# Optimization experiments

Hardware: AMD Instinct MI355X
Metric: run time of the kernel (lower is better)

## Reference

```python
import jax, jax.numpy as jnp
import numpy as np

N = 50000; E = 800000; G = 64
HID = 128; HEADS = 4; HC = HID // HEADS
L = 3; RESID_FREQ = 2
EPS = 1e-5; SLOPE = 0.2


def setup_inputs() -> dict:
    key = jax.random.key(0)
    ks = jax.random.split(key, 16)
    s = 1.0 / np.sqrt(HID)
    f = jnp.float32
    return {
        "x": jax.random.normal(ks[0], (N, HID), f),
        "edge_index": jax.random.randint(ks[1], (2, E), 0, N, dtype=jnp.int32),
        "batch": jnp.sort(jax.random.randint(ks[2], (N,), 0, G, dtype=jnp.int32)),
        "w_in1": jax.random.normal(ks[3], (HID, HID), f) * s,
        "b_in1": jnp.zeros((HID,), f),
        "w_in2": jax.random.normal(ks[4], (HID, HID), f) * s,
        "b_in2": jnp.zeros((HID,), f),
        "gat_w": jax.random.normal(ks[5], (L, HID, HID), f) * s,
        "gat_att_src": jax.random.normal(ks[6], (L, HEADS, HC), f) * s,
        "gat_att_dst": jax.random.normal(ks[7], (L, HEADS, HC), f) * s,
        "gat_b": jnp.zeros((L, HID), f),
        "gcn_w": jax.random.normal(ks[8], (L, HID, HID), f) * s,
        "gcn_b": jnp.zeros((L, HID), f),
        "norm_w": jnp.ones((L, HID), f),
        "norm_b": jnp.zeros((L, HID), f),
        "norm_ms": jnp.ones((L, HID), f),
        "skip_w": jax.random.normal(ks[9], (L, HID, HID), f) * s,
        "skip_b": jnp.zeros((L, HID), f),
        "w_h1": jax.random.normal(ks[10], (HID, HID), f) * s,
        "b_h1": jnp.zeros((HID,), f),
        "w_h2": jax.random.normal(ks[11], (HID, HID // 2), f) * s,
        "b_h2": jnp.zeros((HID // 2,), f),
        "w_h3": jax.random.normal(ks[12], (HID // 2, 1), f) * s,
        "b_h3": jnp.zeros((1,), f),
        "edge_w_param": jnp.ones((1,), f),
    }


def _gat(x, src, dst, w, a_src, a_dst, b):
    # PyG GATConv (eval): lin -> per-edge additive attention -> edge softmax over dst -> scatter-sum
    h = (x @ w).reshape(N, HEADS, HC)
    sc_src = jnp.sum(h * a_src, axis=-1)  # [N, H]
    sc_dst = jnp.sum(h * a_dst, axis=-1)
    alpha = jax.nn.leaky_relu(sc_src[src] + sc_dst[dst], SLOPE)  # [Ef, H]
    amax = jax.ops.segment_max(alpha, dst, num_segments=N)  # every node has a self-loop
    ex = jnp.exp(alpha - amax[dst])
    denom = jax.ops.segment_sum(ex, dst, num_segments=N)
    coef = ex / (denom[dst] + 1e-16)
    out = jax.ops.segment_sum(h[src] * coef[:, :, None], dst, num_segments=N)
    return out.reshape(N, HID) + b


def _gcn(x, src, dst, ew, w, b):
    # PyG GCNConv with improved=True (self-loop weight 2.0 already in ew): sym-normalized SpMM
    deg = jax.ops.segment_sum(ew, dst, num_segments=N)
    dinv = jnp.where(deg > 0, jax.lax.rsqrt(deg), 0.0)
    norm = dinv[src] * ew * dinv[dst]
    h = x @ w
    return jax.ops.segment_sum(h[src] * norm[:, None], dst, num_segments=N) + b


def _graph_norm(x, batch, w, b, ms):
    cnt = jax.ops.segment_sum(jnp.ones((N, 1), x.dtype), batch, num_segments=G)
    cnt = jnp.maximum(cnt, 1.0)
    mean = jax.ops.segment_sum(x, batch, num_segments=G) / cnt
    out = x - mean[batch] * ms
    var = jax.ops.segment_sum(out * out, batch, num_segments=G) / cnt
    return out / jnp.sqrt(var[batch] + EPS) * w + b


def reference(x, edge_index, batch, w_in1, b_in1, w_in2, b_in2, gat_w, gat_att_src,
              gat_att_dst, gat_b, gcn_w, gcn_b, norm_w, norm_b, norm_ms, skip_w,
              skip_b, w_h1, b_h1, w_h2, b_h2, w_h3, b_h3, edge_w_param):
    # undirected: concat reversed edges; then self-loops (added by both GAT and GCN convs)
    loop = jnp.arange(N, dtype=edge_index.dtype)
    src = jnp.concatenate([edge_index[0], edge_index[1], loop])
    dst = jnp.concatenate([edge_index[1], edge_index[0], loop])
    ew = jnp.concatenate([
        edge_w_param[0] * jnp.ones((2 * E,), x.dtype),
        2.0 * jnp.ones((N,), x.dtype),  # improved=True self-loop fill value
    ])
    h = jax.nn.relu(x @ w_in1 + b_in1) @ w_in2 + b_in2
    for i in range(L):
        prev = h
        g1 = _gat(h, src, dst, gat_w[i], gat_att_src[i], gat_att_dst[i], gat_b[i])
        g2 = _gcn(h, src, dst, ew, gcn_w[i], gcn_b[i])
        h = jax.nn.elu(_graph_norm(g1 + g2, batch, norm_w[i], norm_b[i], norm_ms[i]))
        if i % RESID_FREQ == 0:
            h = h + prev @ skip_w[i] + skip_b[i]
    p = jax.nn.relu(h @ w_h1 + b_h1)
    p = jax.nn.relu(p @ w_h2 + b_h2)
    return jax.nn.sigmoid(p @ w_h3 + b_h3).reshape(-1)
```

## Files before the change

kernel.cpp:

```cpp
#include <hip/hip_runtime.h>
#include <hip/hip_fp16.h>

typedef unsigned int uint;
typedef unsigned short ushort;
typedef __attribute__((ext_vector_type(8))) short short8;
typedef __attribute__((ext_vector_type(4))) float f32x4;
typedef __attribute__((ext_vector_type(2))) float f32x2;

#define N_NODES 50000
#define N_EDGES 800000
#define ETOT    (2 * N_EDGES + N_NODES)
#define NG      64
#define NBKT    256
#define MAXB    10240
#define EPB     8192
#define NBK1    ((ETOT + EPB - 1) / EPB)
#define AROW    640

__device__ __forceinline__ short f2bf(float f) {
  uint u = __float_as_uint(f);
  u += 0x7fffu + ((u >> 16) & 1u);
  return (short)(u >> 16);
}
__device__ __forceinline__ float bf2f(short s) {
  return __uint_as_float(((uint)(ushort)s) << 16);
}
__device__ __forceinline__ uint packbf(float a, float b) {
  return (uint)(ushort)f2bf(a) | ((uint)(ushort)f2bf(b) << 16);
}
__device__ __forceinline__ uint pkh2(float a, float b) {
  __half2 h = __floats2half2_rn(a, b);
  return *(uint*)&h;
}
__device__ __forceinline__ float2 uph2(uint u) {
  __half2 h = *(__half2*)&u;
  return __half22float2(h);
}

__global__ __launch_bounds__(256) void bucket_k(const int* __restrict__ ei,
                                                int* __restrict__ gfill,
                                                uint* __restrict__ est) {
  __shared__ int hist[NBKT];
  __shared__ int cursor[NBKT];
  const int tid = threadIdx.x;
  hist[tid] = 0;
  __syncthreads();
  const int e0 = blockIdx.x * EPB;
#pragma unroll 4
  for (int i = 0; i < EPB / 256; ++i) {
    int e = e0 + i * 256 + tid;
    if (e < ETOT) {
      int d;
      if (e < N_EDGES)          d = ei[N_EDGES + e];
      else if (e < 2 * N_EDGES) d = ei[e - N_EDGES];
      else                      d = e - 2 * N_EDGES;
      atomicAdd(&hist[d >> 8], 1);
    }
  }
  __syncthreads();
  cursor[tid] = atomicAdd(&gfill[tid], hist[tid]);
  __syncthreads();
#pragma unroll 4
  for (int i = 0; i < EPB / 256; ++i) {
    int e = e0 + i * 256 + tid;
    if (e < ETOT) {
      int s, d, fl = 0;
      if (e < N_EDGES)          { s = ei[e];           d = ei[N_EDGES + e]; }
      else if (e < 2 * N_EDGES) { s = ei[e];           d = ei[e - N_EDGES]; }
      else                      { s = e - 2 * N_EDGES; d = s; fl = 1; }
      int b = d >> 8;
      int slot = atomicAdd(&cursor[b], 1);
      est[(size_t)b * MAXB + slot] = (uint)s | ((uint)(d & 255) << 16) | ((uint)fl << 24);
    }
  }
}

__global__ __launch_bounds__(256) void bktscan_k(const int* __restrict__ gfill,
                                                 int* __restrict__ bktbase) {
  __shared__ int wsum[4];
  int tid = threadIdx.x, lane = tid & 63, wid = tid >> 6;
  int v = gfill[tid];
  int x = v;
#pragma unroll
  for (int d = 1; d < 64; d <<= 1) {
    int t = __shfl_up(x, d, 64);
    if (lane >= d) x += t;
  }
  if (lane == 63) wsum[wid] = x;
  __syncthreads();
  int woff = 0;
#pragma unroll
  for (int j = 0; j < 4; ++j) if (j < wid) woff += wsum[j];
  bktbase[tid] = woff + x - v;
}

__global__ __launch_bounds__(256) void group_k(const int* __restrict__ gfill,
                                               const int* __restrict__ bktbase,
                                               const uint* __restrict__ est,
                                               const float* __restrict__ ewp,
                                               int* __restrict__ csrc,
                                               int* __restrict__ rbeg,
                                               int* __restrict__ rend,
                                               float* __restrict__ dinv) {
  __shared__ int hist[NBKT];
  __shared__ int cursor[NBKT];
  __shared__ int wsum[4];
  const int b = blockIdx.x;
  const int tid = threadIdx.x;
  const int cnt = gfill[b];
  const int gb = bktbase[b];
  hist[tid] = 0;
  __syncthreads();
  const uint* basep = est + (size_t)b * MAXB;
  for (int i = tid; i < cnt; i += 256)
    atomicAdd(&hist[(basep[i] >> 16) & 255], 1);
  __syncthreads();
  int v = hist[tid];
  int lane = tid & 63, wid = tid >> 6;
  int x = v;
#pragma unroll
  for (int d = 1; d < 64; d <<= 1) {
    int t = __shfl_up(x, d, 64);
    if (lane >= d) x += t;
  }
  if (lane == 63) wsum[wid] = x;
  __syncthreads();
  int woff = 0;
#pragma unroll
  for (int j = 0; j < 4; ++j) if (j < wid) woff += wsum[j];
  int excl = woff + x - v;
  cursor[tid] = excl;
  int node = b * 256 + tid;
  if (node < N_NODES) {
    rbeg[node] = gb + excl;
    rend[node] = gb + excl + v;
    float deg = ewp[0] * (float)(v - 1) + 2.0f;
    dinv[node] = (deg > 0.f) ? rsqrtf(deg) : 0.f;
  }
  __syncthreads();
  for (int i = tid; i < cnt; i += 256) {
    uint en = basep[i];
    int dlow = (en >> 16) & 255;
    int slot = atomicAdd(&cursor[dlow], 1);
    csrc[gb + slot] = (int)(en & 0xffffu) | (int)((en >> 24) << 31);
  }
}

__global__ __launch_bounds__(128) void gcnt_k(const int* __restrict__ batch,
                                              int* __restrict__ gcnt) {
  __shared__ int lb[NG + 1];
  int g = threadIdx.x;
  if (g <= NG) {
    int lo = 0, hi = N_NODES;
    while (lo < hi) {
      int mid = (lo + hi) >> 1;
      if (batch[mid] < g) lo = mid + 1; else hi = mid;
    }
    lb[g] = lo;
  }
  __syncthreads();
  if (g < NG) gcnt[g] = lb[g + 1] - lb[g];
}

__global__ __launch_bounds__(256) void convx_k(const float* __restrict__ x,
                                               short* __restrict__ xb) {
  int i = (blockIdx.x * 256 + threadIdx.x) * 4;
  float4 v = *(const float4*)(x + i);
  *(uint2*)(xb + i) = make_uint2(packbf(v.x, v.y), packbf(v.z, v.w));
}

__global__ __launch_bounds__(256) void prep_k(const float* __restrict__ w_in1,
                                              const float* __restrict__ w_in2,
                                              const float* __restrict__ gat_w,
                                              const float* __restrict__ gcn_w,
                                              const float* __restrict__ skip_w,
                                              const float* __restrict__ w_h1,
                                              const float* __restrict__ w_h2,
                                              short* __restrict__ WT0,
                                              short* __restrict__ WT1,
                                              short* __restrict__ WTL2,
                                              short* __restrict__ WTS,
                                              short* __restrict__ WTH1,
                                              short* __restrict__ WTH2) {
  int mat = blockIdx.x >> 2, qr = blockIdx.x & 3;
  const float* src; short* dst; int ncol = 128, dstride = 128, doff = 0;
  switch (mat) {
    case 0:  src = w_in1; dst = WT0; break;
    case 1:  src = w_in2; dst = WT1; break;
    case 2: case 3: case 4:
      src = gat_w + (size_t)(mat - 2) * 16384; dst = WTL2 + (size_t)(mat - 2) * 32768;
      dstride = 256; break;
    case 5: case 6: case 7:
      src = gcn_w + (size_t)(mat - 5) * 16384; dst = WTL2 + (size_t)(mat - 5) * 32768;
      dstride = 256; doff = 128; break;
    case 8:  src = skip_w;             dst = WTS;         break;
    case 9:  src = skip_w + 2 * 16384; dst = WTS + 16384; break;
    case 10: src = w_h1; dst = WTH1; break;
    default: src = w_h2; dst = WTH2; ncol = 64; break;
  }
  int total = 128 * ncol, chunk = total / 4;
  for (int d = qr * chunk + threadIdx.x; d < (qr + 1) * chunk; d += 256) {
    int col = d >> 7, k = d & 127;
    dst[col * dstride + doff + k] = f2bf(src[k * ncol + col]);
  }
}

__global__ __launch_bounds__(256) void attprep_k(const float* __restrict__ gat_w,
                                                 const float* __restrict__ asrc,
                                                 const float* __restrict__ adst,
                                                 const float* __restrict__ gat_b,
                                                 const float* __restrict__ gcn_b,
                                                 short* __restrict__ ATTW,
                                                 float* __restrict__ BSUM) {
  const int tid = threadIdx.x;
  for (int t = tid; t < 3072; t += 256) {
    int l = t >> 10, rem = t & 1023;
    int r = rem >> 7, k = rem & 127;
    int hd = r & 3;
    const float* av = (r < 4) ? (asrc + l * 128 + hd * 32) : (adst + l * 128 + hd * 32);
    const float* wrow = gat_w + (size_t)l * 16384 + k * 128 + hd * 32;
    float s = 0.f;
#pragma unroll
    for (int c = 0; c < 32; ++c) s = fmaf(wrow[c], av[c], s);
    ATTW[(size_t)l * 2048 + r * 128 + k] = f2bf(s);
  }
  for (int t = tid; t < 3072; t += 256)
    ATTW[(size_t)(t >> 10) * 2048 + 1024 + (t & 1023)] = 0;
  for (int t = tid; t < 384; t += 256) {
    int l = t >> 7, c = t & 127;
    BSUM[t] = gat_b[l * 128 + c] + gcn_b[l * 128 + c];
  }
}

template <int NCOL, int RELU, int ADD, int F32OUT>
__global__ __launch_bounds__(256) void bgemm_k(const short* __restrict__ A,
                                               const short* __restrict__ WT,
                                               const float* __restrict__ bias,
                                               const short* __restrict__ addsrc,
                                               short* __restrict__ outb,
                                               float* __restrict__ outf, int M) {
  constexpr int NT = NCOL / 16;
  const int lane = threadIdx.x & 63;
  const int wid = threadIdx.x >> 6;
  const int mbase = blockIdx.x * 64 + wid * 16;
  const int l15 = lane & 15, q = lane >> 4;
  int arow = mbase + l15; if (arow > M - 1) arow = M - 1;
  const short* ap = A + (size_t)arow * 128 + q * 8;
  const short* bp = WT + (size_t)l15 * 128 + q * 8;
  f32x4 acc[NT];
#pragma unroll
  for (int t = 0; t < NT; ++t) acc[t] = (f32x4)0.f;
#pragma unroll
  for (int c = 0; c < 4; ++c) {
    short8 av = *(const short8*)(ap + c * 32);
#pragma unroll
    for (int t = 0; t < NT; ++t) {
      short8 bv = *(const short8*)(bp + (size_t)t * 16 * 128 + c * 32);
      acc[t] = __builtin_amdgcn_mfma_f32_16x16x32_bf16(av, bv, acc[t], 0, 0, 0);
    }
  }
#pragma unroll
  for (int t = 0; t < NT; ++t) {
    int col = t * 16 + l15;
    float bb = bias ? bias[col] : 0.f;
#pragma unroll
    for (int r = 0; r < 4; ++r) {
      int row = mbase + q * 4 + r;
      if (row < M) {
        float v = acc[t][r] + bb;
        if (ADD) v += bf2f(addsrc[(size_t)row * 128 + col]);
        if (RELU) v = v > 0.f ? v : 0.f;
        if (F32OUT) outf[(size_t)row * NCOL + col] = v;
        else        outb[(size_t)row * NCOL + col] = f2bf(v);
      }
    }
  }
}

__global__ __launch_bounds__(256) void agg_k(const short* __restrict__ h,
                                             const float* __restrict__ sc,
                                             const int* __restrict__ rbeg,
                                             const int* __restrict__ rend,
                                             const int* __restrict__ cs,
                                             const float* __restrict__ dinv,
                                             const float* __restrict__ ewp,
                                             short* __restrict__ A) {
  __shared__ uint4 lco[4][64];
  const int n = blockIdx.x * 4 + (threadIdx.x >> 6);
  const int wv = threadIdx.x >> 6;
  const int l = threadIdx.x & 63;
  const int sub = l >> 5;
  const int f4 = l & 31;
  const float ew0 = ewp[0];
  const float dn = dinv[n];
  const f32x4 sdv = *(const f32x4*)(sc + n * 16 + 4);
  const int beg = rbeg[n], end = rend[n];
  float den[4] = {0.f, 0.f, 0.f, 0.f};
  f32x2 ag[4][2], ac[2];
#pragma unroll
  for (int hd = 0; hd < 4; ++hd) { ag[hd][0] = (f32x2)0.f; ag[hd][1] = (f32x2)0.f; }
  ac[0] = (f32x2)0.f; ac[1] = (f32x2)0.f;

  for (int c0 = beg; c0 < end; c0 += 64) {
    const int nc = min(64, end - c0);
    {
      uint4 w = make_uint4(0u, 0u, 0u, 0u);
      int e = c0 + l;
      if (e < end) {
        int raw = cs[e];
        int s = raw & 0x7fffffff;
        float wt = (raw < 0) ? 2.0f : ew0;
        f32x4 ssv = *(const f32x4*)(sc + (size_t)s * 16);
        float a0 = ssv[0] + sdv[0]; a0 = fmaxf(a0, 0.2f * a0);
        float a1 = ssv[1] + sdv[1]; a1 = fmaxf(a1, 0.2f * a1);
        float a2 = ssv[2] + sdv[2]; a2 = fmaxf(a2, 0.2f * a2);
        float a3 = ssv[3] + sdv[3]; a3 = fmaxf(a3, 0.2f * a3);
        float e0 = __expf(a0), e1 = __expf(a1);
        float e2 = __expf(a2), e3 = __expf(a3);
        den[0] += e0; den[1] += e1; den[2] += e2; den[3] += e3;
        float c2 = dinv[s] * wt * dn;
        __half hc = __float2half(c2);
        w = make_uint4(pkh2(e0, e1), pkh2(e2, e3),
                       (uint)(*(ushort*)&hc) | ((uint)s << 16), 0u);
      }
      lco[wv][l] = w;
    }
    const int pairs = (nc + 1) & ~1;
#pragma unroll 2
    for (int j = sub; j < pairs; j += 2) {
      uint4 cw = lco[wv][j];
      int s = (int)(cw.z >> 16);
      float2 p01 = uph2(cw.x);
      float2 p23 = uph2(cw.y);
      ushort hc = (ushort)(cw.z & 0xffffu);
      float c2 = __half2float(*(__half*)&hc);
      uint2 u = *(const uint2*)(h + (size_t)s * 128 + f4 * 4);
      f32x2 va, vb;
      va.x = __uint_as_float(u.x << 16);
      va.y = __uint_as_float(u.x & 0xffff0000u);
      vb.x = __uint_as_float(u.y << 16);
      vb.y = __uint_as_float(u.y & 0xffff0000u);
      f32x2 cc;
      cc.x = p01.x; cc.y = p01.x;
      ag[0][0] += cc * va; ag[0][1] += cc * vb;
      cc.x = p01.y; cc.y = p01.y;
      ag[1][0] += cc * va; ag[1][1] += cc * vb;
      cc.x = p23.x; cc.y = p23.x;
      ag[2][0] += cc * va; ag[2][1] += cc * vb;
      cc.x = p23.y; cc.y = p23.y;
      ag[3][0] += cc * va; ag[3][1] += cc * vb;
      cc.x = c2; cc.y = c2;
      ac[0] += cc * va; ac[1] += cc * vb;
    }
  }

#pragma unroll
  for (int off = 1; off < 64; off <<= 1) {
    den[0] += __shfl_xor(den[0], off, 64);
    den[1] += __shfl_xor(den[1], off, 64);
    den[2] += __shfl_xor(den[2], off, 64);
    den[3] += __shfl_xor(den[3], off, 64);
  }
#pragma unroll
  for (int hd = 0; hd < 4; ++hd)
#pragma unroll
    for (int i = 0; i < 2; ++i) {
      f32x2 t = ag[hd][i];
      t.x += __shfl_xor(t.x, 32, 64);
      t.y += __shfl_xor(t.y, 32, 64);
      ag[hd][i] = t;
    }
#pragma unroll
  for (int i = 0; i < 2; ++i) {
    f32x2 t = ac[i];
    t.x += __shfl_xor(t.x, 32, 64);
    t.y += __shfl_xor(t.y, 32, 64);
    ac[i] = t;
  }

  float inv[4] = {1.0f / (den[0] + 1e-16f), 1.0f / (den[1] + 1e-16f),
                  1.0f / (den[2] + 1e-16f), 1.0f / (den[3] + 1e-16f)};
  short* base = A + (size_t)n * AROW;
  if (sub == 0) {
#pragma unroll
    for (int hd = 0; hd < 2; ++hd) {
      float iv = inv[hd];
      *(uint2*)(base + hd * 128 + f4 * 4) =
          make_uint2(packbf(ag[hd][0].x * iv, ag[hd][0].y * iv),
                     packbf(ag[hd][1].x * iv, ag[hd][1].y * iv));
    }
    *(uint2*)(base + 512 + f4 * 4) =
        make_uint2(packbf(ac[0].x, ac[0].y), packbf(ac[1].x, ac[1].y));
  } else {
#pragma unroll
    for (int hd = 2; hd < 4; ++hd) {
      float iv = inv[hd];
      *(uint2*)(base + hd * 128 + f4 * 4) =
          make_uint2(packbf(ag[hd][0].x * iv, ag[hd][0].y * iv),
                     packbf(ag[hd][1].x * iv, ag[hd][1].y * iv));
    }
  }
}

__global__ __launch_bounds__(256) void aggproj_k(const short* A,
                                                 const short* __restrict__ WT,
                                                 const float* __restrict__ bsum,
                                                 short* GB, int M) {
  const int lane = threadIdx.x & 63;
  const int wid = threadIdx.x >> 6;
  const int mbase = blockIdx.x * 64 + wid * 16;
  const int l15 = lane & 15, q = lane >> 4;
  int arow = mbase + l15; if (arow > M - 1) arow = M - 1;
  const short* ap = A + (size_t)arow * AROW + q * 8;
  const short* bp = WT + (size_t)l15 * 256 + q * 8;
  f32x4 acc[8];
#pragma unroll
  for (int t = 0; t < 8; ++t) acc[t] = (f32x4)0.f;
  short8 avg[4];
#pragma unroll
  for (int c = 0; c < 4; ++c) avg[c] = *(const short8*)(ap + 512 + c * 32);
#pragma unroll
  for (int hd = 0; hd < 4; ++hd) {
    short8 avh[4];
#pragma unroll
    for (int c = 0; c < 4; ++c) avh[c] = *(const short8*)(ap + hd * 128 + c * 32);
#pragma unroll
    for (int tt = 0; tt < 2; ++tt) {
      int t = hd * 2 + tt;
      const short* bpt = bp + (size_t)t * 16 * 256;
#pragma unroll
      for (int c = 0; c < 4; ++c) {
        short8 bv = *(const short8*)(bpt + c * 32);
        acc[t] = __builtin_amdgcn_mfma_f32_16x16x32_bf16(avh[c], bv, acc[t], 0, 0, 0);
      }
#pragma unroll
      for (int c = 0; c < 4; ++c) {
        short8 bv = *(const short8*)(bpt + 128 + c * 32);
        acc[t] = __builtin_amdgcn_mfma_f32_16x16x32_bf16(avg[c], bv, acc[t], 0, 0, 0);
      }
    }
  }
#pragma unroll
  for (int t = 0; t < 8; ++t) {
    int col = t * 16 + l15;
    float bb = bsum[col];
#pragma unroll
    for (int r = 0; r < 4; ++r) {
      int row = mbase + q * 4 + r;
      if (row < M) GB[(size_t)row * AROW + col] = f2bf(acc[t][r] + bb);
    }
  }
}

__global__ __launch_bounds__(256) void stats_k(const short* __restrict__ gb,
                                               const int* __restrict__ batch,
                                               float* __restrict__ gsum) {
  int c2 = threadIdx.x & 63;
  int qr = threadIdx.x >> 6;
  int nb = blockIdx.x * 16;
  float s0 = 0.f, s1 = 0.f, q0 = 0.f, q1 = 0.f;
  int curb = -1;
  for (int i = qr; i < 16; i += 4) {
    int n = nb + i;
    int b = batch[n];
    if (b != curb) {
      if (curb >= 0) {
        atomicAdd(&gsum[curb * 256 + 2 * c2], s0);
        atomicAdd(&gsum[curb * 256 + 2 * c2 + 1], s1);
        atomicAdd(&gsum[curb * 256 + 128 + 2 * c2], q0);
        atomicAdd(&gsum[curb * 256 + 128 + 2 * c2 + 1], q1);
      }
      curb = b; s0 = s1 = q0 = q1 = 0.f;
    }
    uint u = *(const uint*)(gb + (size_t)n * AROW + 2 * c2);
    float v0 = __uint_as_float(u << 16);
    float v1 = __uint_as_float(u & 0xffff0000u);
    s0 += v0; q0 = fmaf(v0, v0, q0);
    s1 += v1; q1 = fmaf(v1, v1, q1);
  }
  if (curb >= 0) {
    atomicAdd(&gsum[curb * 256 + 2 * c2], s0);
    atomicAdd(&gsum[curb * 256 + 2 * c2 + 1], s1);
    atomicAdd(&gsum[curb * 256 + 128 + 2 * c2], q0);
    atomicAdd(&gsum[curb * 256 + 128 + 2 * c2 + 1], q1);
  }
}

__global__ __launch_bounds__(256) void normelu_k(const short* __restrict__ gb,
                                                 const int* __restrict__ batch,
                                                 const float* __restrict__ gsum,
                                                 const int* __restrict__ gcnt,
                                                 const float* __restrict__ nw,
                                                 const float* __restrict__ nb_,
                                                 const float* __restrict__ nms,
                                                 short* __restrict__ outb) {
  int n = blockIdx.x * 4 + (threadIdx.x >> 6);
  int c2 = threadIdx.x & 63;
  int b = batch[n];
  float cntf = fmaxf((float)gcnt[b], 1.0f);
  float cinv = 1.0f / cntf;
  uint u = *(const uint*)(gb + (size_t)n * AROW + 2 * c2);
  float o[2];
#pragma unroll
  for (int k = 0; k < 2; ++k) {
    int c = 2 * c2 + k;
    float mean = gsum[b * 256 + c] * cinv;
    float msq  = gsum[b * 256 + 128 + c] * cinv;
    float ms = nms[c];
    float var = fmaxf(msq - (2.0f * ms - ms * ms) * mean * mean, 0.f);
    float v = (k == 0) ? __uint_as_float(u << 16) : __uint_as_float(u & 0xffff0000u);
    float t = (v - mean * ms) * rsqrtf(var + 1e-5f) * nw[c] + nb_[c];
    o[k] = (t > 0.f) ? t : (__expf(t) - 1.0f);
  }
  *(uint*)(outb + (size_t)n * 128 + 2 * c2) = packbf(o[0], o[1]);
}

__global__ __launch_bounds__(256) void head3_k(const short* __restrict__ p2,
                                               const float* __restrict__ w3,
                                               const float* __restrict__ b3,
                                               float* __restrict__ out) {
  int n = blockIdx.x * 4 + (threadIdx.x >> 6);
  int k = threadIdx.x & 63;
  float v = bf2f(p2[(size_t)n * 64 + k]) * w3[k];
#pragma unroll
  for (int off = 32; off; off >>= 1) v += __shfl_down(v, off, 64);
  if (k == 0) out[n] = 1.0f / (1.0f + __expf(-(v + b3[0])));
}

extern "C" void kernel_launch(void* const* d_in, const int* in_sizes, int n_in,
                              void* d_out, int out_size, void* d_ws, size_t ws_size,
                              hipStream_t stream) {
  const float* x      = (const float*)d_in[0];
  const int*   ei     = (const int*)d_in[1];
  const int*   batch  = (const int*)d_in[2];
  const float* w_in1  = (const float*)d_in[3];
  const float* b_in1  = (const float*)d_in[4];
  const float* w_in2  = (const float*)d_in[5];
  const float* b_in2  = (const float*)d_in[6];
  const float* gat_w  = (const float*)d_in[7];
  const float* gat_as = (const float*)d_in[8];
  const float* gat_ad = (const float*)d_in[9];
  const float* gat_b  = (const float*)d_in[10];
  const float* gcn_w  = (const float*)d_in[11];
  const float* gcn_b  = (const float*)d_in[12];
  const float* norm_w = (const float*)d_in[13];
  const float* norm_b = (const float*)d_in[14];
  const float* norm_ms= (const float*)d_in[15];
  const float* skip_w = (const float*)d_in[16];
  const float* skip_b = (const float*)d_in[17];
  const float* w_h1   = (const float*)d_in[18];
  const float* b_h1   = (const float*)d_in[19];
  const float* w_h2   = (const float*)d_in[20];
  const float* b_h2   = (const float*)d_in[21];
  const float* w_h3   = (const float*)d_in[22];
  const float* b_h3   = (const float*)d_in[23];
  const float* ewp    = (const float*)d_in[24];
  float* out = (float*)d_out;

  char* p = (char*)d_ws;
  const size_t NBH = (size_t)N_NODES * 128 * sizeof(short);
  short* B0   = (short*)p; p += NBH;
  short* B1   = (short*)p; p += NBH;
  short* NRM  = (short*)p; p += NBH;
  short* MEGA = (short*)p; p += (size_t)N_NODES * AROW * sizeof(short);
  short* GB   = MEGA;
  uint*  EST  = (uint*)MEGA;
  float* SC   = (float*)p; p += (size_t)N_NODES * 16 * sizeof(float);
  int*   CSRC = (int*)p;   p += (size_t)ETOT * sizeof(int);
  int*   RBEG = (int*)p;   p += (size_t)N_NODES * sizeof(int);
  int*   REND = (int*)p;   p += (size_t)N_NODES * sizeof(int);
  char*  zbase = p;
  int*   GFILL= (int*)p;   p += (size_t)NBKT * sizeof(int);
  float* GSUM = (float*)p; p += (size_t)3 * NG * 256 * sizeof(float);
  size_t znb  = (size_t)((char*)p - zbase);
  int*   BKTB = (int*)p;   p += (size_t)NBKT * sizeof(int);
  int*   GCNT = (int*)p;   p += (size_t)NG * sizeof(int);
  float* DINV = (float*)p; p += (size_t)N_NODES * sizeof(float);
  short* WT0  = (short*)p; p += 16384 * sizeof(short);
  short* WT1  = (short*)p; p += 16384 * sizeof(short);
  short* WTL2 = (short*)p; p += 3 * 32768 * sizeof(short);
  short* WTS  = (short*)p; p += 2 * 16384 * sizeof(short);
  short* WTH1 = (short*)p; p += 16384 * sizeof(short);
  short* WTH2 = (short*)p; p += 8192 * sizeof(short);
  short* ATTW = (short*)p; p += 3 * 2048 * sizeof(short);
  float* BSUM = (float*)p; p += 3 * 128 * sizeof(float);

  const int GB_ = (N_NODES + 63) / 64;

  hipMemsetAsync(zbase, 0, znb, stream);
  bucket_k<<<NBK1, 256, 0, stream>>>(ei, GFILL, EST);
  bktscan_k<<<1, 256, 0, stream>>>(GFILL, BKTB);
  group_k<<<196, 256, 0, stream>>>(GFILL, BKTB, EST, ewp, CSRC, RBEG, REND, DINV);
  gcnt_k<<<1, 128, 0, stream>>>(batch, GCNT);
  convx_k<<<(N_NODES * 128) / 1024, 256, 0, stream>>>(x, B0);
  prep_k<<<48, 256, 0, stream>>>(w_in1, w_in2, gat_w, gcn_w, skip_w, w_h1, w_h2,
                                 WT0, WT1, WTL2, WTS, WTH1, WTH2);
  attprep_k<<<1, 256, 0, stream>>>(gat_w, gat_as, gat_ad, gat_b, gcn_b, ATTW, BSUM);

  bgemm_k<128, 1, 0, 0><<<GB_, 256, 0, stream>>>(B0, WT0, b_in1, nullptr, B1, nullptr, N_NODES);
  bgemm_k<128, 0, 0, 0><<<GB_, 256, 0, stream>>>(B1, WT1, b_in2, nullptr, B0, nullptr, N_NODES);

  short* h = B0;
  for (int i = 0; i < 3; ++i) {
    short* hn = (h == B0) ? B1 : B0;
    float* gsum_i = GSUM + (size_t)i * NG * 256;
    bgemm_k<16, 0, 0, 1><<<GB_, 256, 0, stream>>>(h, ATTW + (size_t)i * 2048,
                                                  nullptr, nullptr, nullptr, SC, N_NODES);
    agg_k<<<N_NODES / 4, 256, 0, stream>>>(h, SC, RBEG, REND, CSRC, DINV, ewp, MEGA);
    aggproj_k<<<GB_, 256, 0, stream>>>(MEGA, WTL2 + (size_t)i * 32768,
                                       BSUM + i * 128, GB, N_NODES);
    stats_k<<<N_NODES / 16, 256, 0, stream>>>(GB, batch, gsum_i);
    if (i == 1) {
      normelu_k<<<N_NODES / 4, 256, 0, stream>>>(GB, batch, gsum_i, GCNT,
          norm_w + (size_t)i * 128, norm_b + (size_t)i * 128, norm_ms + (size_t)i * 128,
          hn);
    } else {
      normelu_k<<<N_NODES / 4, 256, 0, stream>>>(GB, batch, gsum_i, GCNT,
          norm_w + (size_t)i * 128, norm_b + (size_t)i * 128, norm_ms + (size_t)i * 128,
          NRM);
      const short* wts = WTS + (size_t)(i == 0 ? 0 : 1) * 16384;
      bgemm_k<128, 0, 1, 0><<<GB_, 256, 0, stream>>>(h, wts, skip_b + (size_t)i * 128,
                                                     NRM, hn, nullptr, N_NODES);
    }
    h = hn;
  }

  bgemm_k<128, 1, 0, 0><<<GB_, 256, 0, stream>>>(h, WTH1, b_h1, nullptr, B0, nullptr, N_NODES);
  bgemm_k<64, 1, 0, 0><<<GB_, 256, 0, stream>>>(B0, WTH2, b_h2, nullptr, MEGA, nullptr, N_NODES);
  head3_k<<<N_NODES / 4, 256, 0, stream>>>(MEGA, w_h3, b_h3, out);
}
```

Baseline: 878.9 us.

## Fuse bucket scan, input conversion, and graph-norm into neighboring kernels

Removes the single-block bucket scan kernel by having each group_k block reduce the preceding bucket counts itself. Drops the separate fp32-to-bf16 input conversion by letting the first GEMM read fp32 rows and pack them to bf16 on the fly. On residual layers, the graph-norm plus ELU is computed inside the skip GEMM epilogue instead of writing and re-reading an intermediate buffer. This cuts launches and memory traffic, at the cost of per-element normalization math and scattered gsum/batch loads in the GEMM epilogue.

```diff
diff --git a/kernel.cpp b/kernel.cpp
--- a/kernel.cpp
+++ b/kernel.cpp
@@ -75,27 +75,7 @@
   }
 }
 
-__global__ __launch_bounds__(256) void bktscan_k(const int* __restrict__ gfill,
-                                                 int* __restrict__ bktbase) {
-  __shared__ int wsum[4];
-  int tid = threadIdx.x, lane = tid & 63, wid = tid >> 6;
-  int v = gfill[tid];
-  int x = v;
-#pragma unroll
-  for (int d = 1; d < 64; d <<= 1) {
-    int t = __shfl_up(x, d, 64);
-    if (lane >= d) x += t;
-  }
-  if (lane == 63) wsum[wid] = x;
-  __syncthreads();
-  int woff = 0;
-#pragma unroll
-  for (int j = 0; j < 4; ++j) if (j < wid) woff += wsum[j];
-  bktbase[tid] = woff + x - v;
-}
-
 __global__ __launch_bounds__(256) void group_k(const int* __restrict__ gfill,
-                                               const int* __restrict__ bktbase,
                                                const uint* __restrict__ est,
                                                const float* __restrict__ ewp,
                                                int* __restrict__ csrc,
@@ -105,18 +85,25 @@
   __shared__ int hist[NBKT];
   __shared__ int cursor[NBKT];
   __shared__ int wsum[4];
+  __shared__ int bsum[4];
   const int b = blockIdx.x;
   const int tid = threadIdx.x;
+  const int lane = tid & 63, wid = tid >> 6;
   const int cnt = gfill[b];
-  const int gb = bktbase[b];
+  {
+    int vv = (tid < b) ? gfill[tid] : 0;
+#pragma unroll
+    for (int off = 32; off; off >>= 1) vv += __shfl_xor(vv, off, 64);
+    if (lane == 0) bsum[wid] = vv;
+  }
   hist[tid] = 0;
   __syncthreads();
+  const int gb = bsum[0] + bsum[1] + bsum[2] + bsum[3];
   const uint* basep = est + (size_t)b * MAXB;
   for (int i = tid; i < cnt; i += 256)
     atomicAdd(&hist[(basep[i] >> 16) & 255], 1);
   __syncthreads();
   int v = hist[tid];
-  int lane = tid & 63, wid = tid >> 6;
   int x = v;
 #pragma unroll
   for (int d = 1; d < 64; d <<= 1) {
@@ -160,13 +147,6 @@
   }
   __syncthreads();
   if (g < NG) gcnt[g] = lb[g + 1] - lb[g];
-}
-
-__global__ __launch_bounds__(256) void convx_k(const float* __restrict__ x,
-                                               short* __restrict__ xb) {
-  int i = (blockIdx.x * 256 + threadIdx.x) * 4;
-  float4 v = *(const float4*)(x + i);
-  *(uint2*)(xb + i) = make_uint2(packbf(v.x, v.y), packbf(v.z, v.w));
 }
 
 __global__ __launch_bounds__(256) void prep_k(const float* __restrict__ w_in1,
@@ -232,11 +212,18 @@
   }
 }
 
-template <int NCOL, int RELU, int ADD, int F32OUT>
+template <int NCOL, int RELU, int F32OUT, int AF32, int NORM>
 __global__ __launch_bounds__(256) void bgemm_k(const short* __restrict__ A,
+                                               const float* __restrict__ Af,
                                                const short* __restrict__ WT,
                                                const float* __restrict__ bias,
-                                               const short* __restrict__ addsrc,
+                                               const short* __restrict__ gb_,
+                                               const int* __restrict__ batch,
+                                               const int* __restrict__ gcnt,
+                                               const float* __restrict__ gsum,
+                                               const float* __restrict__ nw,
+                                               const float* __restrict__ nb_,
+                                               const float* __restrict__ nms,
                                                short* __restrict__ outb,
                                                float* __restrict__ outf, int M) {
   constexpr int NT = NCOL / 16;
@@ -245,14 +232,24 @@
   const int mbase = blockIdx.x * 64 + wid * 16;
   const int l15 = lane & 15, q = lane >> 4;
   int arow = mbase + l15; if (arow > M - 1) arow = M - 1;
-  const short* ap = A + (size_t)arow * 128 + q * 8;
   const short* bp = WT + (size_t)l15 * 128 + q * 8;
   f32x4 acc[NT];
 #pragma unroll
   for (int t = 0; t < NT; ++t) acc[t] = (f32x4)0.f;
 #pragma unroll
   for (int c = 0; c < 4; ++c) {
-    short8 av = *(const short8*)(ap + c * 32);
+    short8 av;
+    if (AF32) {
+      const float* apf = Af + (size_t)arow * 128 + q * 8 + c * 32;
+      float4 fa = *(const float4*)apf;
+      float4 fb = *(const float4*)(apf + 4);
+      uint2 lo = make_uint2(packbf(fa.x, fa.y), packbf(fa.z, fa.w));
+      uint2 hi = make_uint2(packbf(fb.x, fb.y), packbf(fb.z, fb.w));
+      uint4 all = make_uint4(lo.x, lo.y, hi.x, hi.y);
+      av = *(short8*)&all;
+    } else {
+      av = *(const short8*)(A + (size_t)arow * 128 + q * 8 + c * 32);
+    }
 #pragma unroll
     for (int t = 0; t < NT; ++t) {
       short8 bv = *(const short8*)(bp + (size_t)t * 16 * 128 + c * 32);
@@ -268,7 +265,18 @@
       int row = mbase + q * 4 + r;
       if (row < M) {
         float v = acc[t][r] + bb;
-        if (ADD) v += bf2f(addsrc[(size_t)row * 128 + col]);
+        if (NORM) {
+          int b = batch[row];
+          float cinv = 1.0f / fmaxf((float)gcnt[b], 1.0f);
+          float mean = gsum[b * 256 + col] * cinv;
+          float msq  = gsum[b * 256 + 128 + col] * cinv;
+          float ms = nms[col];
+          float var = fmaxf(msq - (2.0f * ms - ms * ms) * mean * mean, 0.f);
+          float g = bf2f(gb_[(size_t)row * AROW + col]);
+          float tn = (g - mean * ms) * rsqrtf(var + 1e-5f) * nw[col] + nb_[col];
+          tn = (tn > 0.f) ? tn : (__expf(tn) - 1.0f);
+          v += tn;
+        }
         if (RELU) v = v > 0.f ? v : 0.f;
         if (F32OUT) outf[(size_t)row * NCOL + col] = v;
         else        outb[(size_t)row * NCOL + col] = f2bf(v);
@@ -561,7 +569,6 @@
   const size_t NBH = (size_t)N_NODES * 128 * sizeof(short);
   short* B0   = (short*)p; p += NBH;
   short* B1   = (short*)p; p += NBH;
-  short* NRM  = (short*)p; p += NBH;
   short* MEGA = (short*)p; p += (size_t)N_NODES * AROW * sizeof(short);
   short* GB   = MEGA;
   uint*  EST  = (uint*)MEGA;
@@ -573,7 +580,6 @@
   int*   GFILL= (int*)p;   p += (size_t)NBKT * sizeof(int);
   float* GSUM = (float*)p; p += (size_t)3 * NG * 256 * sizeof(float);
   size_t znb  = (size_t)((char*)p - zbase);
-  int*   BKTB = (int*)p;   p += (size_t)NBKT * sizeof(int);
   int*   GCNT = (int*)p;   p += (size_t)NG * sizeof(int);
   float* DINV = (float*)p; p += (size_t)N_NODES * sizeof(float);
   short* WT0  = (short*)p; p += 16384 * sizeof(short);
@@ -586,46 +592,50 @@
   float* BSUM = (float*)p; p += 3 * 128 * sizeof(float);
 
   const int GB_ = (N_NODES + 63) / 64;
+  const short* nullb = nullptr;
 
   hipMemsetAsync(zbase, 0, znb, stream);
   bucket_k<<<NBK1, 256, 0, stream>>>(ei, GFILL, EST);
-  bktscan_k<<<1, 256, 0, stream>>>(GFILL, BKTB);
-  group_k<<<196, 256, 0, stream>>>(GFILL, BKTB, EST, ewp, CSRC, RBEG, REND, DINV);
+  group_k<<<196, 256, 0, stream>>>(GFILL, EST, ewp, CSRC, RBEG, REND, DINV);
   gcnt_k<<<1, 128, 0, stream>>>(batch, GCNT);
-  convx_k<<<(N_NODES * 128) / 1024, 256, 0, stream>>>(x, B0);
   prep_k<<<48, 256, 0, stream>>>(w_in1, w_in2, gat_w, gcn_w, skip_w, w_h1, w_h2,
                                  WT0, WT1, WTL2, WTS, WTH1, WTH2);
   attprep_k<<<1, 256, 0, stream>>>(gat_w, gat_as, gat_ad, gat_b, gcn_b, ATTW, BSUM);
 
-  bgemm_k<128, 1, 0, 0><<<GB_, 256, 0, stream>>>(B0, WT0, b_in1, nullptr, B1, nullptr, N_NODES);
-  bgemm_k<128, 0, 0, 0><<<GB_, 256, 0, stream>>>(B1, WT1, b_in2, nullptr, B0, nullptr, N_NODES);
+  bgemm_k<128, 1, 0, 1, 0><<<GB_, 256, 0, stream>>>(nullb, x, WT0, b_in1,
+      nullb, nullptr, nullptr, nullptr, nullptr, nullptr, nullptr, B1, nullptr, N_NODES);
+  bgemm_k<128, 0, 0, 0, 0><<<GB_, 256, 0, stream>>>(B1, nullptr, WT1, b_in2,
+      nullb, nullptr, nullptr, nullptr, nullptr, nullptr, nullptr, B0, nullptr, N_NODES);
 
   short* h = B0;
   for (int i = 0; i < 3; ++i) {
     short* hn = (h == B0) ? B1 : B0;
     float* gsum_i = GSUM + (size_t)i * NG * 256;
-    bgemm_k<16, 0, 0, 1><<<GB_, 256, 0, stream>>>(h, ATTW + (size_t)i * 2048,
-                                                  nullptr, nullptr, nullptr, SC, N_NODES);
+    const float* nw  = norm_w  + (size_t)i * 128;
+    const float* nb  = norm_b  + (size_t)i * 128;
+    const float* nms = norm_ms + (size_t)i * 128;
+    bgemm_k<16, 0, 1, 0, 0><<<GB_, 256, 0, stream>>>(h, nullptr,
+        ATTW + (size_t)i * 2048, nullptr, nullb, nullptr, nullptr, nullptr,
+        nullptr, nullptr, nullptr, nullptr, SC, N_NODES);
     agg_k<<<N_NODES / 4, 256, 0, stream>>>(h, SC, RBEG, REND, CSRC, DINV, ewp, MEGA);
     aggproj_k<<<GB_, 256, 0, stream>>>(MEGA, WTL2 + (size_t)i * 32768,
                                        BSUM + i * 128, GB, N_NODES);
     stats_k<<<N_NODES / 16, 256, 0, stream>>>(GB, batch, gsum_i);
     if (i == 1) {
       normelu_k<<<N_NODES / 4, 256, 0, stream>>>(GB, batch, gsum_i, GCNT,
-          norm_w + (size_t)i * 128, norm_b + (size_t)i * 128, norm_ms + (size_t)i * 128,
-          hn);
+                                                 nw, nb, nms, hn);
     } else {
-      normelu_k<<<N_NODES / 4, 256, 0, stream>>>(GB, batch, gsum_i, GCNT,
-          norm_w + (size_t)i * 128, norm_b + (size_t)i * 128, norm_ms + (size_t)i * 128,
-          NRM);
       const short* wts = WTS + (size_t)(i == 0 ? 0 : 1) * 16384;
-      bgemm_k<128, 0, 1, 0><<<GB_, 256, 0, stream>>>(h, wts, skip_b + (size_t)i * 128,
-                                                     NRM, hn, nullptr, N_NODES);
+      bgemm_k<128, 0, 0, 0, 1><<<GB_, 256, 0, stream>>>(h, nullptr, wts,
+          skip_b + (size_t)i * 128, GB, batch, GCNT, gsum_i, nw, nb, nms,
+          hn, nullptr, N_NODES);
     }
     h = hn;
   }
 
-  bgemm_k<128, 1, 0, 0><<<GB_, 256, 0, stream>>>(h, WTH1, b_h1, nullptr, B0, nullptr, N_NODES);
-  bgemm_k<64, 1, 0, 0><<<GB_, 256, 0, stream>>>(B0, WTH2, b_h2, nullptr, MEGA, nullptr, N_NODES);
+  bgemm_k<128, 1, 0, 0, 0><<<GB_, 256, 0, stream>>>(h, nullptr, WTH1, b_h1,
+      nullb, nullptr, nullptr, nullptr, nullptr, nullptr, nullptr, B0, nullptr, N_NODES);
+  bgemm_k<64, 1, 0, 0, 0><<<GB_, 256, 0, stream>>>(B0, nullptr, WTH2, b_h2,
+      nullb, nullptr, nullptr, nullptr, nullptr, nullptr, nullptr, MEGA, nullptr, N_NODES);
   head3_k<<<N_NODES / 4, 256, 0, stream>>>(MEGA, w_h3, b_h3, out);
 }
```

Measured after the change: 856.0 us. 1.03x faster.
